# Optimization experiments

Measured on AMD Instinct MI355X. Metric: run time of the kernel, lower is better.

Reference implementation:

```python
import jax, jax.numpy as jnp
import numpy as np

B = 262144
NUM_FEA = 256          # input feature dim, split into two towers of 128
HIDDEN = [64, 32, 16]  # tower hidden units
CO_FEA = 32            # 2 * HIDDEN[-1], features entering co-attention
EMB = 8                # per-feature embedding dim
OUT_DIM = 16           # final Dense(16)


def setup_inputs() -> dict:
    key = jax.random.key(0)
    ks = jax.random.split(key, 12)
    mid = NUM_FEA // 2
    def glorot(k, shape):
        fan_in, fan_out = shape[0], shape[1]
        lim = np.sqrt(6.0 / (fan_in + fan_out)).astype(np.float32)
        return jax.random.uniform(k, shape, jnp.float32, -lim, lim)
    return {
        "x": jax.random.normal(ks[0], (B, NUM_FEA), jnp.float32),
        # shared tower (weight_share=True -> only mod_dnn1 is used)
        "W1": glorot(ks[1], (mid, HIDDEN[0])), "b1": jnp.zeros((HIDDEN[0],), jnp.float32),
        "W2": glorot(ks[2], (HIDDEN[0], HIDDEN[1])), "b2": jnp.zeros((HIDDEN[1],), jnp.float32),
        "W3": glorot(ks[3], (HIDDEN[1], HIDDEN[2])), "b3": jnp.zeros((HIDDEN[2],), jnp.float32),
        # 32 per-feature Dense(8) layers on scalar inputs, stacked: weight [32,8], bias [32,8]
        "W_emb": glorot(ks[4], (CO_FEA, EMB)),
        "b_emb": jnp.zeros((CO_FEA, EMB), jnp.float32),
        # bilinear co-attention matrix
        "M": glorot(ks[5], (EMB, EMB)),
        # final Dense(16, relu) for mix='concat'
        "W_out": glorot(ks[6], (CO_FEA, OUT_DIM)),
        "b_out": jnp.zeros((OUT_DIM,), jnp.float32),
    }


def reference(x, W1, b1, W2, b2, W3, b3, W_emb, b_emb, M, W_out, b_out):
    mid = x.shape[1] // 2

    def tower(h):
        h = jax.nn.relu(h @ W1 + b1)
        h = jax.nn.relu(h @ W2 + b2)
        h = jax.nn.relu(h @ W3 + b3)
        return h

    left = tower(x[:, :mid])      # [B,16]
    right = tower(x[:, mid:])     # [B,16] (weight_share=True)
    out = jnp.concatenate([left, right], axis=-1)  # [B,32]

    # 32 tiny Dense(emb) on scalar features, batched: [B,32,1]*[32,8] + [32,8]
    emb = out[:, :, None] * W_emb[None, :, :] + b_emb[None, :, :]  # [B,32,8]
    cmid = out.shape[1] // 2  # 16
    l, r = emb[:, :cmid, :], emb[:, cmid:, :]

    G = jnp.tanh(jnp.einsum('bie,ef,bjf->bij', l, M, r))  # [B,16,16]
    lr = jax.nn.softmax(G.sum(axis=1), axis=-1)           # [B,16]
    rl = jax.nn.softmax(G.sum(axis=2), axis=-1)           # [B,16]
    a = jnp.concatenate([lr, rl], axis=-1)                # [B,32]

    out = out * a
    # mix == 'concat' -> Dense(16, relu)
    return jax.nn.relu(out @ W_out + b_out)               # [B,16]
```

## Files before the change

kernel.cpp:

```cpp
#include <hip/hip_runtime.h>

typedef __attribute__((ext_vector_type(8))) short bf16x8;
typedef __attribute__((ext_vector_type(4))) float f32x4;

#define MFMA16(a, b, c) __builtin_amdgcn_mfma_f32_16x16x32_bf16(a, b, c, 0, 0, 0)

__device__ __forceinline__ unsigned short f2bf(float f) {
    unsigned u = __builtin_bit_cast(unsigned, f);
    u += 0x7FFFu + ((u >> 16) & 1u);
    return (unsigned short)(u >> 16);
}
__device__ __forceinline__ float bf2f(unsigned short h) {
    return __builtin_bit_cast(float, (unsigned)h << 16);
}

__device__ __forceinline__ void split8(const float* v, bf16x8& hi, bf16x8& lo) {
    unsigned* hp = reinterpret_cast<unsigned*>(&hi);
    unsigned* lp = reinterpret_cast<unsigned*>(&lo);
    #pragma unroll
    for (int q = 0; q < 4; ++q) {
        const float a = v[2 * q], b = v[2 * q + 1];
        unsigned hpair;
        asm("v_cvt_pk_bf16_f32 %0, %1, %2" : "=v"(hpair) : "v"(a), "v"(b));
        const float ha = __builtin_bit_cast(float, hpair << 16);
        const float hb = __builtin_bit_cast(float, hpair & 0xFFFF0000u);
        const float ra = a - ha, rb = b - hb;
        unsigned lpair;
        asm("v_cvt_pk_bf16_f32 %0, %1, %2" : "=v"(lpair) : "v"(ra), "v"(rb));
        hp[q] = hpair;
        lp[q] = lpair;
    }
}

__global__ void prep_kernel(const float* __restrict__ W1,
                            const float* __restrict__ W2,
                            const float* __restrict__ W3,
                            const float* __restrict__ W_emb,
                            const float* __restrict__ b_emb,
                            const float* __restrict__ M,
                            float* __restrict__ pqrs,
                            unsigned short* __restrict__ w1h,
                            unsigned short* __restrict__ w1l,
                            unsigned short* __restrict__ wsm) {
    const int t = threadIdx.x;
    const float C2 = 2.8853900817779268f;
    {
        const int j = t >> 4;
        const int i = t & 15;
        float mr[8], mb[8];
        #pragma unroll
        for (int e = 0; e < 8; ++e) {
            float ar = 0.f, ab = 0.f;
            #pragma unroll
            for (int f = 0; f < 8; ++f) {
                const float m = M[e * 8 + f];
                ar = fmaf(m, W_emb[(16 + j) * 8 + f], ar);
                ab = fmaf(m, b_emb[(16 + j) * 8 + f], ab);
            }
            mr[e] = ar; mb[e] = ab;
        }
        float P = 0.f, Q = 0.f, R = 0.f, S = 0.f;
        #pragma unroll
        for (int e = 0; e < 8; ++e) {
            const float lw = W_emb[i * 8 + e];
            const float lb = b_emb[i * 8 + e];
            P = fmaf(lw, mr[e], P);
            Q = fmaf(lw, mb[e], Q);
            R = fmaf(lb, mr[e], R);
            S = fmaf(lb, mb[e], S);
        }
        pqrs[0 * 256 + j * 16 + i] = C2 * P;
        pqrs[1 * 256 + j * 16 + i] = C2 * Q;
        pqrs[2 * 256 + j * 16 + i] = C2 * R;
        pqrs[3 * 256 + j * 16 + i] = C2 * S;
    }
    for (int e = 0; e < 32; ++e) {
        const int idx = t * 32 + e;
        const int i = idx & 7, lane = (idx >> 3) & 63;
        const int n = (idx >> 9) & 3, kt = idx >> 11;
        const int k = kt * 32 + (lane >> 4) * 8 + i;
        const int c = n * 16 + (lane & 15);
        const float v = W1[k * 64 + c];
        const unsigned short h = f2bf(v);
        w1h[idx] = h;
        w1l[idx] = f2bf(v - bf2f(h));
    }
    for (int e = 0; e < 8; ++e) {
        const int idx = t * 8 + e;
        const int i = idx & 7, lane = (idx >> 3) & 63;
        const int n = (idx >> 9) & 1, kt = (idx >> 10) & 1;
        const int k = kt * 32 + (lane >> 4) * 8 + i;
        const int c = n * 16 + (lane & 15);
        const float v = W2[k * 32 + c];
        const unsigned short h = f2bf(v);
        wsm[idx] = h;
        wsm[2048 + idx] = f2bf(v - bf2f(h));
    }
    for (int e = 0; e < 2; ++e) {
        const int idx = t * 2 + e;
        const int i = idx & 7, lane = (idx >> 3) & 63;
        const int k = (lane >> 4) * 8 + i;
        const int c = lane & 15;
        const float v = W3[k * 16 + c];
        const unsigned short h = f2bf(v);
        wsm[4096 + idx] = h;
        wsm[4608 + idx] = f2bf(v - bf2f(h));
    }
}

__global__ __launch_bounds__(256, 3) void fused_kernel(
    const float* __restrict__ x,
    const unsigned short* __restrict__ w1h,
    const unsigned short* __restrict__ w1l,
    const unsigned short* __restrict__ wsm,
    const float* __restrict__ b1, const float* __restrict__ b2,
    const float* __restrict__ b3,
    const float* __restrict__ pqrs,
    const float* __restrict__ W_out, const float* __restrict__ b_out,
    float* __restrict__ y) {
    __shared__ float s_tr[4][16 * 68];
    __shared__ float s_h3[4][64 * 20];

    const int tid = threadIdx.x;
    const int l  = tid & 63;
    const int wv = tid >> 6;
    const int lm = l & 15;
    const int lg = l >> 4;

    const unsigned short* w2h = wsm;
    const unsigned short* w2l = wsm + 2048;
    const unsigned short* w3h = wsm + 4096;
    const unsigned short* w3l = wsm + 4608;

    float b1v[4], b2v[2];
    #pragma unroll
    for (int n = 0; n < 4; ++n) b1v[n] = b1[n * 16 + lm];
    #pragma unroll
    for (int n = 0; n < 2; ++n) b2v[n] = b2[n * 16 + lm];
    const float b3v = b3[lm];

    const long tr0 = (long)blockIdx.x * 256 + wv * 64;
    float* tb  = s_tr[wv];
    float* h3b = s_h3[wv];

    float4 xb[2][8];
    {
        const float* xp = x + (tr0 + lm) * 128 + lg * 8;
        #pragma unroll
        for (int kt = 0; kt < 4; ++kt) {
            xb[0][2 * kt]     = *(const float4*)(xp + kt * 32);
            xb[0][2 * kt + 1] = *(const float4*)(xp + kt * 32 + 4);
        }
    }

    #pragma unroll
    for (int tile = 0; tile < 4; ++tile) {
        const int cur = tile & 1, nxt = cur ^ 1;
        if (tile < 3) {
            const float* xp = x + (tr0 + (tile + 1) * 16 + lm) * 128 + lg * 8;
            #pragma unroll
            for (int kt = 0; kt < 4; ++kt) {
                xb[nxt][2 * kt]     = *(const float4*)(xp + kt * 32);
                xb[nxt][2 * kt + 1] = *(const float4*)(xp + kt * 32 + 4);
            }
        }
        f32x4 acc[4];
        #pragma unroll
        for (int n = 0; n < 4; ++n) acc[n] = f32x4{b1v[n], b1v[n], b1v[n], b1v[n]};
        #pragma unroll
        for (int kt = 0; kt < 4; ++kt) {
            const float4 a = xb[cur][2 * kt], b = xb[cur][2 * kt + 1];
            const float xv[8] = {a.x, a.y, a.z, a.w, b.x, b.y, b.z, b.w};
            bf16x8 xh, xl; split8(xv, xh, xl);
            #pragma unroll
            for (int n = 0; n < 4; ++n) {
                const int fo = ((kt * 4 + n) * 64 + l) * 8;
                const bf16x8 wh = *(const bf16x8*)(w1h + fo);
                const bf16x8 wl = *(const bf16x8*)(w1l + fo);
                acc[n] = MFMA16(xh, wh, acc[n]);
                acc[n] = MFMA16(xl, wh, acc[n]);
                acc[n] = MFMA16(xh, wl, acc[n]);
            }
        }
        #pragma unroll
        for (int n = 0; n < 4; ++n)
            #pragma unroll
            for (int r = 0; r < 4; ++r)
                tb[(lg * 4 + r) * 68 + n * 16 + lm] = fmaxf(acc[n][r], 0.f);
        f32x4 acc2[2];
        #pragma unroll
        for (int n = 0; n < 2; ++n) acc2[n] = f32x4{b2v[n], b2v[n], b2v[n], b2v[n]};
        #pragma unroll
        for (int kt = 0; kt < 2; ++kt) {
            const float* ap = tb + lm * 68 + kt * 32 + lg * 8;
            const float4 h0 = *(const float4*)(ap);
            const float4 h1 = *(const float4*)(ap + 4);
            const float hv[8] = {h0.x, h0.y, h0.z, h0.w, h1.x, h1.y, h1.z, h1.w};
            bf16x8 hh, hl; split8(hv, hh, hl);
            #pragma unroll
            for (int n = 0; n < 2; ++n) {
                const int fo = ((kt * 2 + n) * 64 + l) * 8;
                const bf16x8 wh = *(const bf16x8*)(w2h + fo);
                const bf16x8 wl = *(const bf16x8*)(w2l + fo);
                acc2[n] = MFMA16(hh, wh, acc2[n]);
                acc2[n] = MFMA16(hl, wh, acc2[n]);
                acc2[n] = MFMA16(hh, wl, acc2[n]);
            }
        }
        #pragma unroll
        for (int n = 0; n < 2; ++n)
            #pragma unroll
            for (int r = 0; r < 4; ++r)
                tb[(lg * 4 + r) * 68 + n * 16 + lm] = fmaxf(acc2[n][r], 0.f);
        f32x4 acc3 = f32x4{b3v, b3v, b3v, b3v};
        {
            const float* ap = tb + lm * 68 + lg * 8;
            const float4 h0 = *(const float4*)(ap);
            const float4 h1 = *(const float4*)(ap + 4);
            const float hv[8] = {h0.x, h0.y, h0.z, h0.w, h1.x, h1.y, h1.z, h1.w};
            bf16x8 hh, hl; split8(hv, hh, hl);
            const bf16x8 wh = *(const bf16x8*)(w3h + l * 8);
            const bf16x8 wl = *(const bf16x8*)(w3l + l * 8);
            acc3 = MFMA16(hh, wh, acc3);
            acc3 = MFMA16(hl, wh, acc3);
            acc3 = MFMA16(hh, wl, acc3);
        }
        #pragma unroll
        for (int r = 0; r < 4; ++r)
            h3b[(tile * 16 + lg * 4 + r) * 20 + lm] = fmaxf(acc3[r], 0.f);
    }

    const int p = l & 1;
    float o[16];
    {
        const float4* hp = (const float4*)(h3b + l * 20);
        const float4 t0 = hp[0], t1 = hp[1], t2 = hp[2], t3 = hp[3];
        o[0] = t0.x;  o[1] = t0.y;  o[2] = t0.z;  o[3] = t0.w;
        o[4] = t1.x;  o[5] = t1.y;  o[6] = t1.z;  o[7] = t1.w;
        o[8] = t2.x;  o[9] = t2.y;  o[10] = t2.z; o[11] = t2.w;
        o[12] = t3.x; o[13] = t3.y; o[14] = t3.z; o[15] = t3.w;
    }
    float oL[16], oR[16];
    #pragma unroll
    for (int i = 0; i < 16; ++i) {
        const float oth = __shfl_xor(o[i], 1);
        oL[i] = p ? oth : o[i];
        oR[i] = p ? o[i] : oth;
    }

    float sir[16];
    #pragma unroll
    for (int i = 0; i < 16; ++i) sir[i] = 0.f;
    float sjv[16];
    #pragma unroll
    for (int j = 0; j < 16; ++j) {
        const float r = oR[j];
        const float* __restrict__ Pr = pqrs +       j * 16;
        const float* __restrict__ Qr = pqrs + 256 + j * 16;
        const float* __restrict__ Rr = pqrs + 512 + j * 16;
        const float* __restrict__ Sr = pqrs + 768 + j * 16;
        float accr = 0.f;
        #pragma unroll
        for (int i = 0; i < 16; ++i) {
            const float t1 = fmaf(r, Pr[i], Qr[i]);
            const float t2 = fmaf(r, Rr[i], Sr[i]);
            const float z  = fmaf(oL[i], t1, t2);
            const float e  = __builtin_amdgcn_exp2f(z);
            const float rc = __builtin_amdgcn_rcpf(e + 1.0f);
            accr   += rc;
            sir[i] += rc;
        }
        sjv[j] = accr;
    }
    #pragma unroll
    for (int i = 0; i < 16; ++i) {
        sjv[i] = fmaf(-2.f, sjv[i], 16.f);
        sir[i] = fmaf(-2.f, sir[i], 16.f);
    }

    {
        float mx = sjv[0];
        #pragma unroll
        for (int i = 1; i < 16; ++i) mx = fmaxf(mx, sjv[i]);
        float s = 0.f; float ex[16];
        #pragma unroll
        for (int i = 0; i < 16; ++i) { ex[i] = __expf(sjv[i] - mx); s += ex[i]; }
        const float inv = __builtin_amdgcn_rcpf(s);
        #pragma unroll
        for (int i = 0; i < 16; ++i) oL[i] *= ex[i] * inv;
    }
    {
        float mx = sir[0];
        #pragma unroll
        for (int i = 1; i < 16; ++i) mx = fmaxf(mx, sir[i]);
        float s = 0.f; float ex[16];
        #pragma unroll
        for (int i = 0; i < 16; ++i) { ex[i] = __expf(sir[i] - mx); s += ex[i]; }
        const float inv = __builtin_amdgcn_rcpf(s);
        #pragma unroll
        for (int i = 0; i < 16; ++i) oR[i] *= ex[i] * inv;
    }

    float yv[16];
    #pragma unroll
    for (int oo = 0; oo < 16; ++oo) yv[oo] = b_out[oo];
    #pragma unroll
    for (int c = 0; c < 16; ++c) {
        const float cl = oL[c];
        const float cr = oR[c];
        const float* __restrict__ wl = W_out + c * 16;
        const float* __restrict__ wt = W_out + (16 + c) * 16;
        #pragma unroll
        for (int oo = 0; oo < 16; ++oo) {
            yv[oo] = fmaf(cl, wl[oo], yv[oo]);
            yv[oo] = fmaf(cr, wt[oo], yv[oo]);
        }
    }
    #pragma unroll
    for (int oo = 0; oo < 16; ++oo) yv[oo] = fmaxf(yv[oo], 0.f);

    float4 v0, v1;
    v0.x = p ? yv[8]  : yv[0]; v0.y = p ? yv[9]  : yv[1];
    v0.z = p ? yv[10] : yv[2]; v0.w = p ? yv[11] : yv[3];
    v1.x = p ? yv[12] : yv[4]; v1.y = p ? yv[13] : yv[5];
    v1.z = p ? yv[14] : yv[6]; v1.w = p ? yv[15] : yv[7];
    float* __restrict__ yo = y + ((tr0 >> 1) + (l >> 1)) * 16 + p * 8;
    *reinterpret_cast<float4*>(yo)     = v0;
    *reinterpret_cast<float4*>(yo + 4) = v1;
}

extern "C" void kernel_launch(void* const* d_in, const int* in_sizes, int n_in,
                              void* d_out, int out_size, void* d_ws, size_t ws_size,
                              hipStream_t stream) {
    const float* x     = (const float*)d_in[0];
    const float* W1    = (const float*)d_in[1];
    const float* b1    = (const float*)d_in[2];
    const float* W2    = (const float*)d_in[3];
    const float* b2    = (const float*)d_in[4];
    const float* W3    = (const float*)d_in[5];
    const float* b3    = (const float*)d_in[6];
    const float* W_emb = (const float*)d_in[7];
    const float* b_emb = (const float*)d_in[8];
    const float* M     = (const float*)d_in[9];
    const float* W_out = (const float*)d_in[10];
    const float* b_out = (const float*)d_in[11];
    float* y = (float*)d_out;

    float* pqrs = (float*)d_ws;
    unsigned short* w1h = (unsigned short*)((char*)d_ws + 4096);
    unsigned short* w1l = w1h + 8192;
    unsigned short* wsm = w1l + 8192;

    const int nrows = in_sizes[0] / 256;

    prep_kernel<<<1, 256, 0, stream>>>(W1, W2, W3, W_emb, b_emb, M,
                                       pqrs, w1h, w1l, wsm);
    const int grid = nrows / 128;
    fused_kernel<<<grid, 256, 0, stream>>>(x, w1h, w1l, wsm,
                                           b1, b2, b3, pqrs, W_out, b_out, y);
}
```

Baseline: 141.4 us.

## Split co-attention and output dense work across lane pairs instead of duplicating

Each pair of lanes previously computed the full 16x16 tanh attention grid and the full 16-wide output dense redundantly for the same row. Now each lane computes half of the j columns and half of the output columns, and the partial row/column sums are combined with xor-1 shuffles. The softmax constants are pre-scaled by log2(e) so exp2 replaces __expf. This halves the transcendental and FMA work per lane at the cost of a few extra shuffles and selects.

```diff
diff --git a/kernel.cpp b/kernel.cpp
--- a/kernel.cpp
+++ b/kernel.cpp
@@ -247,18 +247,22 @@
         oL[i] = p ? oth : o[i];
         oR[i] = p ? o[i] : oth;
     }
+    float oRh[8];
+    #pragma unroll
+    for (int jj = 0; jj < 8; ++jj) oRh[jj] = p ? oR[8 + jj] : oR[jj];
 
     float sir[16];
     #pragma unroll
     for (int i = 0; i < 16; ++i) sir[i] = 0.f;
-    float sjv[16];
-    #pragma unroll
-    for (int j = 0; j < 16; ++j) {
-        const float r = oR[j];
-        const float* __restrict__ Pr = pqrs +       j * 16;
-        const float* __restrict__ Qr = pqrs + 256 + j * 16;
-        const float* __restrict__ Rr = pqrs + 512 + j * 16;
-        const float* __restrict__ Sr = pqrs + 768 + j * 16;
+    float sjl[8];
+    const float* __restrict__ pq = pqrs + p * 128;
+    #pragma unroll
+    for (int jj = 0; jj < 8; ++jj) {
+        const float r = oRh[jj];
+        const float* __restrict__ Pr = pq +        jj * 16;
+        const float* __restrict__ Qr = pq + 256  + jj * 16;
+        const float* __restrict__ Rr = pq + 512  + jj * 16;
+        const float* __restrict__ Sr = pq + 768  + jj * 16;
         float accr = 0.f;
         #pragma unroll
         for (int i = 0; i < 16; ++i) {
@@ -270,12 +274,22 @@
             accr   += rc;
             sir[i] += rc;
         }
-        sjv[j] = accr;
-    }
+        sjl[jj] = accr;
+    }
+    #pragma unroll
+    for (int i = 0; i < 16; ++i) sir[i] += __shfl_xor(sir[i], 1);
+    float sjv[16];
+    #pragma unroll
+    for (int jj = 0; jj < 8; ++jj) {
+        const float oth = __shfl_xor(sjl[jj], 1);
+        sjv[jj]     = p ? oth     : sjl[jj];
+        sjv[8 + jj] = p ? sjl[jj] : oth;
+    }
+    const float KA = 23.083120654223414f, KB = 2.8853900817779268f;
     #pragma unroll
     for (int i = 0; i < 16; ++i) {
-        sjv[i] = fmaf(-2.f, sjv[i], 16.f);
-        sir[i] = fmaf(-2.f, sir[i], 16.f);
+        sjv[i] = fmaf(-KB, sjv[i], KA);
+        sir[i] = fmaf(-KB, sir[i], KA);
     }
 
     {
@@ -284,7 +298,7 @@
         for (int i = 1; i < 16; ++i) mx = fmaxf(mx, sjv[i]);
         float s = 0.f; float ex[16];
         #pragma unroll
-        for (int i = 0; i < 16; ++i) { ex[i] = __expf(sjv[i] - mx); s += ex[i]; }
+        for (int i = 0; i < 16; ++i) { ex[i] = __builtin_amdgcn_exp2f(sjv[i] - mx); s += ex[i]; }
         const float inv = __builtin_amdgcn_rcpf(s);
         #pragma unroll
         for (int i = 0; i < 16; ++i) oL[i] *= ex[i] * inv;
@@ -295,35 +309,34 @@
         for (int i = 1; i < 16; ++i) mx = fmaxf(mx, sir[i]);
         float s = 0.f; float ex[16];
         #pragma unroll
-        for (int i = 0; i < 16; ++i) { ex[i] = __expf(sir[i] - mx); s += ex[i]; }
+        for (int i = 0; i < 16; ++i) { ex[i] = __builtin_amdgcn_exp2f(sir[i] - mx); s += ex[i]; }
         const float inv = __builtin_amdgcn_rcpf(s);
         #pragma unroll
         for (int i = 0; i < 16; ++i) oR[i] *= ex[i] * inv;
     }
 
-    float yv[16];
-    #pragma unroll
-    for (int oo = 0; oo < 16; ++oo) yv[oo] = b_out[oo];
+    float yv[8];
+    const float* __restrict__ bo = b_out + p * 8;
+    #pragma unroll
+    for (int oo = 0; oo < 8; ++oo) yv[oo] = bo[oo];
     #pragma unroll
     for (int c = 0; c < 16; ++c) {
         const float cl = oL[c];
         const float cr = oR[c];
-        const float* __restrict__ wl = W_out + c * 16;
-        const float* __restrict__ wt = W_out + (16 + c) * 16;
-        #pragma unroll
-        for (int oo = 0; oo < 16; ++oo) {
+        const float* __restrict__ wl = W_out + c * 16 + p * 8;
+        const float* __restrict__ wt = W_out + (16 + c) * 16 + p * 8;
+        #pragma unroll
+        for (int oo = 0; oo < 8; ++oo) {
             yv[oo] = fmaf(cl, wl[oo], yv[oo]);
             yv[oo] = fmaf(cr, wt[oo], yv[oo]);
         }
     }
-    #pragma unroll
-    for (int oo = 0; oo < 16; ++oo) yv[oo] = fmaxf(yv[oo], 0.f);
 
     float4 v0, v1;
-    v0.x = p ? yv[8]  : yv[0]; v0.y = p ? yv[9]  : yv[1];
-    v0.z = p ? yv[10] : yv[2]; v0.w = p ? yv[11] : yv[3];
-    v1.x = p ? yv[12] : yv[4]; v1.y = p ? yv[13] : yv[5];
-    v1.z = p ? yv[14] : yv[6]; v1.w = p ? yv[15] : yv[7];
+    v0.x = fmaxf(yv[0], 0.f); v0.y = fmaxf(yv[1], 0.f);
+    v0.z = fmaxf(yv[2], 0.f); v0.w = fmaxf(yv[3], 0.f);
+    v1.x = fmaxf(yv[4], 0.f); v1.y = fmaxf(yv[5], 0.f);
+    v1.z = fmaxf(yv[6], 0.f); v1.w = fmaxf(yv[7], 0.f);
     float* __restrict__ yo = y + ((tr0 >> 1) + (l >> 1)) * 16 + p * 8;
     *reinterpret_cast<float4*>(yo)     = v0;
     *reinterpret_cast<float4*>(yo + 4) = v1;
```

After: 192.6 us. 1.36x slower.

## Compute tower layers 2 and 3 with per-lane scalar FMAs instead of split-bf16 MFMA

Applied to the files above, without the earlier changes.

Layer 1 outputs for all 64 rows of each wave are now staged in a padded shared buffer, and each lane computes layers 2 and 3 for its own row with scalar fp32 FMAs. The weights are read from global memory with uniform addresses, and the bf16 hi/lo weight preprocessing for W2 and W3 is dropped. This removes per-tile shared-memory round trips, split8 conversions and the 3-pass MFMA emulation, and it gives exact fp32 for those layers. In exchange it adds about 2.5K scalar FMAs per row plus many scalar weight loads, and the larger shared buffer may lower occupancy.

```diff
diff --git a/kernel.cpp b/kernel.cpp
--- a/kernel.cpp
+++ b/kernel.cpp
@@ -33,15 +33,12 @@
 }
 
 __global__ void prep_kernel(const float* __restrict__ W1,
-                            const float* __restrict__ W2,
-                            const float* __restrict__ W3,
                             const float* __restrict__ W_emb,
                             const float* __restrict__ b_emb,
                             const float* __restrict__ M,
                             float* __restrict__ pqrs,
                             unsigned short* __restrict__ w1h,
-                            unsigned short* __restrict__ w1l,
-                            unsigned short* __restrict__ wsm) {
+                            unsigned short* __restrict__ w1l) {
     const int t = threadIdx.x;
     const float C2 = 2.8853900817779268f;
     {
@@ -85,41 +82,19 @@
         w1h[idx] = h;
         w1l[idx] = f2bf(v - bf2f(h));
     }
-    for (int e = 0; e < 8; ++e) {
-        const int idx = t * 8 + e;
-        const int i = idx & 7, lane = (idx >> 3) & 63;
-        const int n = (idx >> 9) & 1, kt = (idx >> 10) & 1;
-        const int k = kt * 32 + (lane >> 4) * 8 + i;
-        const int c = n * 16 + (lane & 15);
-        const float v = W2[k * 32 + c];
-        const unsigned short h = f2bf(v);
-        wsm[idx] = h;
-        wsm[2048 + idx] = f2bf(v - bf2f(h));
-    }
-    for (int e = 0; e < 2; ++e) {
-        const int idx = t * 2 + e;
-        const int i = idx & 7, lane = (idx >> 3) & 63;
-        const int k = (lane >> 4) * 8 + i;
-        const int c = lane & 15;
-        const float v = W3[k * 16 + c];
-        const unsigned short h = f2bf(v);
-        wsm[4096 + idx] = h;
-        wsm[4608 + idx] = f2bf(v - bf2f(h));
-    }
 }
 
 __global__ __launch_bounds__(256, 3) void fused_kernel(
     const float* __restrict__ x,
     const unsigned short* __restrict__ w1h,
     const unsigned short* __restrict__ w1l,
-    const unsigned short* __restrict__ wsm,
-    const float* __restrict__ b1, const float* __restrict__ b2,
-    const float* __restrict__ b3,
+    const float* __restrict__ b1,
+    const float* __restrict__ W2, const float* __restrict__ b2,
+    const float* __restrict__ W3, const float* __restrict__ b3,
     const float* __restrict__ pqrs,
     const float* __restrict__ W_out, const float* __restrict__ b_out,
     float* __restrict__ y) {
-    __shared__ float s_tr[4][16 * 68];
-    __shared__ float s_h3[4][64 * 20];
+    __shared__ float s_h1[4][64 * 65];
 
     const int tid = threadIdx.x;
     const int l  = tid & 63;
@@ -127,21 +102,12 @@
     const int lm = l & 15;
     const int lg = l >> 4;
 
-    const unsigned short* w2h = wsm;
-    const unsigned short* w2l = wsm + 2048;
-    const unsigned short* w3h = wsm + 4096;
-    const unsigned short* w3l = wsm + 4608;
-
-    float b1v[4], b2v[2];
+    float b1v[4];
     #pragma unroll
     for (int n = 0; n < 4; ++n) b1v[n] = b1[n * 16 + lm];
-    #pragma unroll
-    for (int n = 0; n < 2; ++n) b2v[n] = b2[n * 16 + lm];
-    const float b3v = b3[lm];
 
     const long tr0 = (long)blockIdx.x * 256 + wv * 64;
-    float* tb  = s_tr[wv];
-    float* h3b = s_h3[wv];
+    float* h1b = s_h1[wv];
 
     float4 xb[2][8];
     {
@@ -186,60 +152,35 @@
         for (int n = 0; n < 4; ++n)
             #pragma unroll
             for (int r = 0; r < 4; ++r)
-                tb[(lg * 4 + r) * 68 + n * 16 + lm] = fmaxf(acc[n][r], 0.f);
-        f32x4 acc2[2];
-        #pragma unroll
-        for (int n = 0; n < 2; ++n) acc2[n] = f32x4{b2v[n], b2v[n], b2v[n], b2v[n]};
-        #pragma unroll
-        for (int kt = 0; kt < 2; ++kt) {
-            const float* ap = tb + lm * 68 + kt * 32 + lg * 8;
-            const float4 h0 = *(const float4*)(ap);
-            const float4 h1 = *(const float4*)(ap + 4);
-            const float hv[8] = {h0.x, h0.y, h0.z, h0.w, h1.x, h1.y, h1.z, h1.w};
-            bf16x8 hh, hl; split8(hv, hh, hl);
-            #pragma unroll
-            for (int n = 0; n < 2; ++n) {
-                const int fo = ((kt * 2 + n) * 64 + l) * 8;
-                const bf16x8 wh = *(const bf16x8*)(w2h + fo);
-                const bf16x8 wl = *(const bf16x8*)(w2l + fo);
-                acc2[n] = MFMA16(hh, wh, acc2[n]);
-                acc2[n] = MFMA16(hl, wh, acc2[n]);
-                acc2[n] = MFMA16(hh, wl, acc2[n]);
-            }
-        }
-        #pragma unroll
-        for (int n = 0; n < 2; ++n)
-            #pragma unroll
-            for (int r = 0; r < 4; ++r)
-                tb[(lg * 4 + r) * 68 + n * 16 + lm] = fmaxf(acc2[n][r], 0.f);
-        f32x4 acc3 = f32x4{b3v, b3v, b3v, b3v};
-        {
-            const float* ap = tb + lm * 68 + lg * 8;
-            const float4 h0 = *(const float4*)(ap);
-            const float4 h1 = *(const float4*)(ap + 4);
-            const float hv[8] = {h0.x, h0.y, h0.z, h0.w, h1.x, h1.y, h1.z, h1.w};
-            bf16x8 hh, hl; split8(hv, hh, hl);
-            const bf16x8 wh = *(const bf16x8*)(w3h + l * 8);
-            const bf16x8 wl = *(const bf16x8*)(w3l + l * 8);
-            acc3 = MFMA16(hh, wh, acc3);
-            acc3 = MFMA16(hl, wh, acc3);
-            acc3 = MFMA16(hh, wl, acc3);
-        }
-        #pragma unroll
-        for (int r = 0; r < 4; ++r)
-            h3b[(tile * 16 + lg * 4 + r) * 20 + lm] = fmaxf(acc3[r], 0.f);
-    }
+                h1b[(tile * 16 + lg * 4 + r) * 65 + n * 16 + lm] =
+                    fmaxf(acc[n][r], 0.f);
+    }
+
+    float h2[32];
+    #pragma unroll
+    for (int j = 0; j < 32; ++j) h2[j] = b2[j];
+    const float* __restrict__ h1r = h1b + l * 65;
+    #pragma unroll 8
+    for (int k = 0; k < 64; ++k) {
+        const float hk = h1r[k];
+        const float* __restrict__ wr = W2 + k * 32;
+        #pragma unroll
+        for (int j = 0; j < 32; ++j) h2[j] = fmaf(hk, wr[j], h2[j]);
+    }
+    float o[16];
+    #pragma unroll
+    for (int j = 0; j < 16; ++j) o[j] = b3[j];
+    #pragma unroll
+    for (int k = 0; k < 32; ++k) {
+        const float hk = fmaxf(h2[k], 0.f);
+        const float* __restrict__ wr = W3 + k * 16;
+        #pragma unroll
+        for (int j = 0; j < 16; ++j) o[j] = fmaf(hk, wr[j], o[j]);
+    }
+    #pragma unroll
+    for (int j = 0; j < 16; ++j) o[j] = fmaxf(o[j], 0.f);
 
     const int p = l & 1;
-    float o[16];
-    {
-        const float4* hp = (const float4*)(h3b + l * 20);
-        const float4 t0 = hp[0], t1 = hp[1], t2 = hp[2], t3 = hp[3];
-        o[0] = t0.x;  o[1] = t0.y;  o[2] = t0.z;  o[3] = t0.w;
-        o[4] = t1.x;  o[5] = t1.y;  o[6] = t1.z;  o[7] = t1.w;
-        o[8] = t2.x;  o[9] = t2.y;  o[10] = t2.z; o[11] = t2.w;
-        o[12] = t3.x; o[13] = t3.y; o[14] = t3.z; o[15] = t3.w;
-    }
     float oL[16], oR[16];
     #pragma unroll
     for (int i = 0; i < 16; ++i) {
@@ -349,13 +290,11 @@
     float* pqrs = (float*)d_ws;
     unsigned short* w1h = (unsigned short*)((char*)d_ws + 4096);
     unsigned short* w1l = w1h + 8192;
-    unsigned short* wsm = w1l + 8192;
 
     const int nrows = in_sizes[0] / 256;
 
-    prep_kernel<<<1, 256, 0, stream>>>(W1, W2, W3, W_emb, b_emb, M,
-                                       pqrs, w1h, w1l, wsm);
+    prep_kernel<<<1, 256, 0, stream>>>(W1, W_emb, b_emb, M, pqrs, w1h, w1l);
     const int grid = nrows / 128;
-    fused_kernel<<<grid, 256, 0, stream>>>(x, w1h, w1l, wsm,
-                                           b1, b2, b3, pqrs, W_out, b_out, y);
-}
+    fused_kernel<<<grid, 256, 0, stream>>>(x, w1h, w1l, b1, W2, b2, W3, b3,
+                                           pqrs, W_out, b_out, y);
+}
```

New measurement: 178.7 us. 1.26x slower.
